# Kernel optimization log

Measured on AMD Instinct MI355X. Metric: run time of the kernel, lower is better.

Reference implementation:

```python
import jax, jax.numpy as jnp
import numpy as np
from jax import lax

B, T, N, C = 32, 32, 64, 64          # batch, window, num_series, inter_dim
GRU_H, QK, HOR = 64, 32, 12          # gru_dim, qk_dim, prediction_horizon
KS = (3, 5, 7)                       # temporal kernel per block (3 + 2*i)


def setup_inputs() -> dict:
    key = jax.random.key(0)
    ks = jax.random.split(key, 32)
    rn = lambda k, shape, s=0.05: jax.random.normal(k, shape, jnp.float32) * s
    inp = {"x": jax.random.normal(ks[0], (B, T, N), jnp.float32)}
    # x_to_inter_dim: Conv1d(1, C, kernel_size=1) == scalar * w + b
    inp["w_x2i"] = rn(ks[1], (C,)); inp["b_x2i"] = rn(ks[2], (C,))
    # latentCorrelation GRU (input_size=1, hidden=GRU_H), gate order r,z,n
    inp["gru_wih"] = rn(ks[3], (3 * GRU_H, 1)); inp["gru_whh"] = rn(ks[4], (3 * GRU_H, GRU_H))
    inp["gru_bih"] = rn(ks[5], (3 * GRU_H,)); inp["gru_bhh"] = rn(ks[6], (3 * GRU_H,))
    inp["wq_w"] = rn(ks[7], (QK, GRU_H)); inp["wq_b"] = rn(ks[8], (QK,))
    inp["wk_w"] = rn(ks[9], (QK, GRU_H)); inp["wk_b"] = rn(ks[10], (QK,))
    # per block: T independent GCNConvs (theta + bias), one temporal Conv1d
    for i, k_ in enumerate(KS):
        inp[f"gcn_w{i}"] = rn(ks[11 + 4 * i], (T, C, C))
        inp[f"gcn_b{i}"] = rn(ks[12 + 4 * i], (T, C))
        inp[f"conv_w{i}"] = rn(ks[13 + 4 * i], (C, C, k_))
        inp[f"conv_b{i}"] = rn(ks[14 + 4 * i], (C,))
    inp["lout_w"] = rn(ks[25], (N * HOR, T * N * C), 0.01)
    inp["lout_b"] = rn(ks[26], (N * HOR,))
    return inp


def _forward(x, w_x2i, b_x2i, gru_wih, gru_whh, gru_bih, gru_bhh,
             wq_w, wq_b, wk_w, wk_b,
             gcn_w0, gcn_b0, conv_w0, conv_b0,
             gcn_w1, gcn_b1, conv_w1, conv_b1,
             gcn_w2, gcn_b2, conv_w2, conv_b2,
             lout_w, lout_b):
    xs = jnp.transpose(x, (1, 0, 2))  # (T, B, N) time-major

    # --- latentCorrelation: one GRU run over all B*N series at once ---
    def gru_step(h, xt):  # h: (B,N,GRU_H), xt: (B,N)
        gi = xt[..., None] * gru_wih[:, 0] + gru_bih           # (B,N,3H)
        gh = h @ gru_whh.T + gru_bhh                           # (B,N,3H)
        r = jax.nn.sigmoid(gi[..., :GRU_H] + gh[..., :GRU_H])
        z = jax.nn.sigmoid(gi[..., GRU_H:2 * GRU_H] + gh[..., GRU_H:2 * GRU_H])
        n = jnp.tanh(gi[..., 2 * GRU_H:] + r * gh[..., 2 * GRU_H:])
        return (1.0 - z) * n + z * h, None

    h0 = jnp.zeros((B, N, GRU_H), x.dtype)
    hT, _ = lax.scan(gru_step, h0, xs)                         # (B,N,GRU_H)
    Q = hT @ wq_w.T + wq_b                                     # (B,N,QK)
    K = hT @ wk_w.T + wk_b
    Wadj = jax.nn.softmax(jnp.einsum('bnq,bmq->bnm', Q, K) / jnp.sqrt(jnp.float32(QK)), axis=2)

    # GCN symmetric norm on the dense complete graph; edge (src=i, tgt=j) has
    # weight Wadj[b,i,j]; degree is per-target (column) sum.
    deg = Wadj.sum(axis=1)                                     # (B,N)
    dinv = jnp.where(deg > 0, 1.0 / jnp.sqrt(deg), 0.0)
    What = dinv[:, :, None] * Wadj * dinv[:, None, :]          # (B,N,N)

    # x_to_inter_dim (1x1 conv) applied per timestep
    feats = xs[..., None] * w_x2i + b_x2i                      # (T,B,N,C)

    for gw, gb, cw, cb, k_ in ((gcn_w0, gcn_b0, conv_w0, conv_b0, 3),
                               (gcn_w1, gcn_b1, conv_w1, conv_b1, 5),
                               (gcn_w2, gcn_b2, conv_w2, conv_b2, 7)):
        xw = jnp.einsum('tbnc,tcd->tbnd', feats, gw)           # per-timestep theta
        agg = jnp.einsum('bij,tbid->tbjd', What, xw) + gb[:, None, None, :]
        seq = jnp.transpose(agg, (1, 2, 3, 0)).reshape(B * N, C, T)
        p = k_ // 2
        conv = lax.conv_general_dilated(seq, cw, (1,), [(p, p)],
                                        dimension_numbers=('NCH', 'OIH', 'NCH'))
        conv = conv + cb[None, :, None]
        conv = jnp.where(conv >= 0, conv, 0.01 * conv)         # LeakyReLU (dropout p=0)
        feats = jnp.transpose(conv.reshape(B, N, C, T), (3, 0, 1, 2))

    # stack(x_list, dim=2).view(B*N, C*T).view(B, -1) -> (B, N*C*T) feature order (n,c,t)
    flat = jnp.transpose(feats, (1, 2, 3, 0)).reshape(B, N * C * T)
    out = flat @ lout_w.T + lout_b                             # (B, N*HOR)
    return out.reshape(B, HOR, N)


def reference(x, w_x2i, b_x2i, gru_wih, gru_whh, gru_bih, gru_bhh,
              wq_w, wq_b, wk_w, wk_b,
              gcn_w0, gcn_b0, conv_w0, conv_b0,
              gcn_w1, gcn_b1, conv_w1, conv_b1,
              gcn_w2, gcn_b2, conv_w2, conv_b2,
              lout_w, lout_b):
    return _forward(x, w_x2i, b_x2i, gru_wih, gru_whh, gru_bih, gru_bhh,
                    wq_w, wq_b, wk_w, wk_b,
                    gcn_w0, gcn_b0, conv_w0, conv_b0,
                    gcn_w1, gcn_b1, conv_w1, conv_b1,
                    gcn_w2, gcn_b2, conv_w2, conv_b2,
                    lout_w, lout_b)
```

## Files before the change

kernel.cpp:

```cpp
#include <hip/hip_runtime.h>
#include <hip/hip_bf16.h>

#define BB 32
#define TT 32
#define NN 64
#define CC 64
#define HH 64
#define QKD 32
#define HOR 12
#define OUTD (NN*HOR)
#define KFLAT (NN*CC*TT)

typedef __attribute__((ext_vector_type(4))) float f32x4;
typedef __attribute__((ext_vector_type(8))) short s16x8;
typedef unsigned short ush;

static __device__ __forceinline__ ush f2bf(float f) {
    unsigned u = __float_as_uint(f);
    unsigned r = (u + 0x7FFFu + ((u >> 16) & 1u)) >> 16;
    return (ush)r;
}
static __device__ __forceinline__ float bf2f(ush h) {
    return __uint_as_float(((unsigned)h) << 16);
}
static __device__ __forceinline__ void split8(const float* f, uint4& hi, uint4& lo) {
    unsigned hh[8], ll[8];
    #pragma unroll
    for (int i = 0; i < 8; ++i) {
        ush h = f2bf(f[i]);
        float hf = bf2f(h);
        hh[i] = h;
        ll[i] = f2bf(f[i] - hf);
    }
    hi = make_uint4(hh[0] | (hh[1] << 16), hh[2] | (hh[3] << 16),
                    hh[4] | (hh[5] << 16), hh[6] | (hh[7] << 16));
    lo = make_uint4(ll[0] | (ll[1] << 16), ll[2] | (ll[3] << 16),
                    ll[4] | (ll[5] << 16), ll[6] | (ll[7] << 16));
}
static __device__ __forceinline__ void gl2lds16(const void* gsrc, void* ldst) {
    __builtin_amdgcn_global_load_lds(
        (const __attribute__((address_space(1))) unsigned int*)gsrc,
        (__attribute__((address_space(3))) unsigned int*)ldst, 16, 0, 0);
}

__global__ __launch_bounds__(256) void prep_gru_kernel(
    const float* __restrict__ x, const float* __restrict__ wih,
    const float* __restrict__ whh, const float* __restrict__ bih,
    const float* __restrict__ bhh, float* __restrict__ hT,
    const float* __restrict__ gw0, const float* __restrict__ wx, const float* __restrict__ bx,
    float* __restrict__ u, float* __restrict__ v,
    const float* __restrict__ gw1, ush* __restrict__ g1h, ush* __restrict__ g1l,
    const float* __restrict__ gw2, ush* __restrict__ g2h, ush* __restrict__ g2l,
    const float* __restrict__ cw1, ush* __restrict__ c1h, ush* __restrict__ c1l,
    const float* __restrict__ cw2, ush* __restrict__ c2h, ush* __restrict__ c2l,
    const float* __restrict__ cw3, ush* __restrict__ c3h, ush* __restrict__ c3l,
    const float* __restrict__ lb, float* __restrict__ out)
{
    __shared__ __align__(16) char smem[17408];
    int bid = blockIdx.x, tid = threadIdx.x;

    if (bid < 32) {
        float (*pu)[64] = (float(*)[64])smem;
        float (*pv)[64] = (float(*)[64])(smem + 1024);
        int t = bid, d = tid & 63, cq = tid >> 6;
        float su = 0.f, sv = 0.f;
        for (int c = cq*16; c < cq*16 + 16; ++c) {
            float gv = gw0[t*4096 + c*64 + d];
            su += wx[c]*gv; sv += bx[c]*gv;
        }
        pu[cq][d] = su; pv[cq][d] = sv;
        __syncthreads();
        if (tid < 64) {
            u[t*64 + tid] = pu[0][tid]+pu[1][tid]+pu[2][tid]+pu[3][tid];
            v[t*64 + tid] = pv[0][tid]+pv[1][tid]+pv[2][tid]+pv[3][tid];
        }
    } else if (bid < 96) {
        const float* gw = (bid < 64) ? gw1 : gw2;
        ush* hi = (bid < 64) ? g1h : g2h;
        ush* lo = (bid < 64) ? g1l : g2l;
        int t = (bid < 64) ? bid - 32 : bid - 64;
        for (int idx = tid; idx < 4096; idx += 256) {
            int d = idx >> 6, c = idx & 63;
            float val = gw[t*4096 + c*64 + d];
            ush h = f2bf(val);
            hi[t*4096 + idx] = h;
            lo[t*4096 + idx] = f2bf(val - bf2f(h));
        }
    } else if (bid < 224) {
        const float* cw; ush *hi, *lo; int KW, co;
        if (bid < 160) { cw = cw2; hi = c2h; lo = c2l; KW = 5; co = bid - 96; }
        else           { cw = cw3; hi = c3h; lo = c3l; KW = 7; co = bid - 160; }
        int K = KW*64;
        for (int idx = tid; idx < K; idx += 256) {
            int ka = idx >> 6, ci = idx & 63;
            float val = cw[(size_t)(co*64 + ci)*KW + ka];
            ush h = f2bf(val);
            hi[(size_t)co*K + idx] = h;
            lo[(size_t)co*K + idx] = f2bf(val - bf2f(h));
        }
    } else if (bid < 288) {
        const float* cw = cw1; ush *hi = c1h, *lo = c1l; int KW = 3, co = bid - 224;
        int K = KW*64;
        for (int idx = tid; idx < K; idx += 256) {
            int ka = idx >> 6, ci = idx & 63;
            float val = cw[(size_t)(co*64 + ci)*KW + ka];
            ush h = f2bf(val);
            hi[(size_t)co*K + idx] = h;
            lo[(size_t)co*K + idx] = f2bf(val - bf2f(h));
        }
    } else if (bid < 384) {
        int idx = (bid - 288)*256 + tid;
        out[idx] = lb[idx % OUTD];
    }
    __syncthreads();

    {
        float (*hbuf)[64] = (float(*)[64])smem;
        float4* part = (float4*)(smem + 1024);
        int w = tid >> 6, j = tid & 63;
        float Wreg[3][16];
        #pragma unroll
        for (int g = 0; g < 3; ++g)
            #pragma unroll
            for (int q = 0; q < 4; ++q) {
                float4 wv = *(const float4*)&whh[(g*64 + j)*64 + w*16 + q*4];
                Wreg[g][q*4+0] = wv.x; Wreg[g][q*4+1] = wv.y;
                Wreg[g][q*4+2] = wv.z; Wreg[g][q*4+3] = wv.w;
            }
        hbuf[w][j] = 0.0f;
        int gs0 = bid * 4;
        int b = gs0 >> 6, n0 = gs0 & 63;
        float wih_r = wih[j], wih_z = wih[64+j], wih_n = wih[128+j];
        float bi_r = bih[j], bi_z = bih[64+j], bi_n = bih[128+j];
        float bh_r = bhh[j], bh_z = bhh[64+j], bh_n = bhh[128+j];
        __syncthreads();
        float hreg = 0.0f;
        for (int t = 0; t < TT; ++t) {
            float p[3][4];
            #pragma unroll
            for (int g = 0; g < 3; ++g)
                #pragma unroll
                for (int s = 0; s < 4; ++s) p[g][s] = 0.f;
            #pragma unroll
            for (int s = 0; s < 4; ++s) {
                #pragma unroll
                for (int q = 0; q < 4; ++q) {
                    const float4 hv = *(const float4*)&hbuf[s][w*16 + q*4];
                    #pragma unroll
                    for (int g = 0; g < 3; ++g) {
                        p[g][s] += hv.x*Wreg[g][q*4]   + hv.y*Wreg[g][q*4+1]
                                 + hv.z*Wreg[g][q*4+2] + hv.w*Wreg[g][q*4+3];
                    }
                }
            }
            #pragma unroll
            for (int s = 0; s < 4; ++s)
                part[(w*4 + s)*64 + j] = make_float4(p[0][s], p[1][s], p[2][s], 0.f);
            __syncthreads();
            float4 q0 = part[(0*4 + w)*64 + j];
            float4 q1 = part[(1*4 + w)*64 + j];
            float4 q2 = part[(2*4 + w)*64 + j];
            float4 q3 = part[(3*4 + w)*64 + j];
            float gr = bh_r + q0.x + q1.x + q2.x + q3.x;
            float gz = bh_z + q0.y + q1.y + q2.y + q3.y;
            float gn = bh_n + q0.z + q1.z + q2.z + q3.z;
            float xt = x[(b*TT + t)*NN + n0 + w];
            float r = 1.f/(1.f+__expf(-(xt*wih_r + bi_r + gr)));
            float z = 1.f/(1.f+__expf(-(xt*wih_z + bi_z + gz)));
            float nn_ = tanhf(xt*wih_n + bi_n + r*gn);
            float hnew = (1.f - z)*nn_ + z*hreg;
            hreg = hnew;
            hbuf[w][j] = hnew;
            __syncthreads();
        }
        hT[(gs0 + w)*64 + j] = hreg;
    }
}

__global__ __launch_bounds__(256) void attn_kernel(
    const float* __restrict__ hT, const float* __restrict__ wq_w,
    const float* __restrict__ wq_b, const float* __restrict__ wk_w,
    const float* __restrict__ wk_b,
    ush* __restrict__ whT_hi, ush* __restrict__ whT_lo)
{
    __shared__ float hs[64][64];
    __shared__ float Qs[64][33], Ks[64][33];
    __shared__ float S[64][65];
    __shared__ float pd[4][64];
    __shared__ float dinv[64];
    int b = blockIdx.x, tid = threadIdx.x;
    for (int idx = tid; idx < 64*64; idx += 256) hs[idx>>6][idx&63] = hT[b*4096 + idx];
    __syncthreads();
    for (int idx = tid; idx < 64*32; idx += 256) {
        int n_ = idx >> 5, q = idx & 31;
        float accq = wq_b[q], acck = wk_b[q];
        #pragma unroll 8
        for (int h_ = 0; h_ < 64; ++h_) {
            float hv = hs[n_][h_];
            accq += hv * wq_w[q*64 + h_];
            acck += hv * wk_w[q*64 + h_];
        }
        Qs[n_][q] = accq; Ks[n_][q] = acck;
    }
    __syncthreads();
    const float scale = 0.17677669529663687f;
    for (int idx = tid; idx < 64*64; idx += 256) {
        int n_ = idx >> 6, m = idx & 63;
        float acc = 0.f;
        #pragma unroll 8
        for (int q = 0; q < 32; ++q) acc += Qs[n_][q]*Ks[m][q];
        S[n_][m] = acc * scale;
    }
    __syncthreads();
    {
        int r = tid >> 2, q = tid & 3;
        float mx = -1e30f;
        #pragma unroll
        for (int m = 0; m < 16; ++m) mx = fmaxf(mx, S[r][q*16+m]);
        mx = fmaxf(mx, __shfl_xor(mx, 1));
        mx = fmaxf(mx, __shfl_xor(mx, 2));
        float sum = 0.f;
        float e[16];
        #pragma unroll
        for (int m = 0; m < 16; ++m) { e[m] = __expf(S[r][q*16+m]-mx); sum += e[m]; }
        sum += __shfl_xor(sum, 1);
        sum += __shfl_xor(sum, 2);
        float inv = 1.f/sum;
        #pragma unroll
        for (int m = 0; m < 16; ++m) S[r][q*16+m] = e[m]*inv;
    }
    __syncthreads();
    {
        int c = tid & 63, rq = tid >> 6;
        float d = 0.f;
        #pragma unroll
        for (int i = 0; i < 16; ++i) d += S[rq*16 + i][c];
        pd[rq][c] = d;
    }
    __syncthreads();
    if (tid < 64) {
        float d = pd[0][tid]+pd[1][tid]+pd[2][tid]+pd[3][tid];
        dinv[tid] = (d > 0.f) ? 1.0f/sqrtf(d) : 0.f;
    }
    __syncthreads();
    for (int idx = tid; idx < 64*64; idx += 256) {
        int jj = idx >> 6, ii = idx & 63;
        float val = dinv[ii]*S[ii][jj]*dinv[jj];
        ush h = f2bf(val);
        whT_hi[b*4096 + idx] = h;
        whT_lo[b*4096 + idx] = f2bf(val - bf2f(h));
    }
}

template<bool FIRST>
__global__ __launch_bounds__(256) void gcn_mfma(
    const float* __restrict__ fin,
    const ush* __restrict__ gwT_hi, const ush* __restrict__ gwT_lo,
    const float* __restrict__ u, const float* __restrict__ v,
    const ush* __restrict__ whT_hi, const ush* __restrict__ whT_lo,
    const float* __restrict__ gb, float* __restrict__ o)
{
    __shared__ __align__(16) ush ft_hi[64][64], ft_lo[64][64];
    __shared__ __align__(16) ush xsT_hi[64][64], xsT_lo[64][64];
    __shared__ float x_l[64];
    int tb = blockIdx.x, t = tb >> 5, b = tb & 31;
    int tid = threadIdx.x;
    int w = tid >> 6, l = tid & 63, lm = l & 15, ld = l >> 4;

    if (FIRST) {
        if (tid < 64) x_l[tid] = fin[(b*TT + t)*NN + tid];
        __syncthreads();
        int d = tid >> 2, nq = tid & 3;
        float ud = u[t*64 + d], vd = v[t*64 + d];
        float vals[16];
        #pragma unroll
        for (int i = 0; i < 16; ++i) vals[i] = x_l[nq*16 + i]*ud + vd;
        #pragma unroll
        for (int h = 0; h < 2; ++h) {
            uint4 hi, lo; split8(&vals[h*8], hi, lo);
            int un = (nq*2 + h) ^ (d & 7);
            *(uint4*)&xsT_hi[d][un*8] = hi;
            *(uint4*)&xsT_lo[d][un*8] = lo;
        }
        __syncthreads();
    } else {
        {
            int row = tid >> 2, c0 = (tid & 3) * 16;
            const float* src = fin + (size_t)tb*4096 + row*64 + c0;
            float f8a[8], f8b[8];
            *(float4*)f8a = *(const float4*)src;       *(float4*)(f8a+4) = *(const float4*)(src+4);
            *(float4*)f8b = *(const float4*)(src+8);   *(float4*)(f8b+4) = *(const float4*)(src+12);
            uint4 hi, lo;
            split8(f8a, hi, lo);
            int u0 = ((c0>>3)) ^ (row & 7);
            *(uint4*)&ft_hi[row][u0*8] = hi; *(uint4*)&ft_lo[row][u0*8] = lo;
            split8(f8b, hi, lo);
            int u1 = ((c0>>3)+1) ^ (row & 7);
            *(uint4*)&ft_hi[row][u1*8] = hi; *(uint4*)&ft_lo[row][u1*8] = lo;
        }
        __syncthreads();
        f32x4 acc[4];
        #pragma unroll
        for (int ct = 0; ct < 4; ++ct) acc[ct] = (f32x4){0.f,0.f,0.f,0.f};
        #pragma unroll
        for (int kc = 0; kc < 2; ++kc) {
            int nrow = w*16 + lm;
            int ux = (kc*4 + ld) ^ (nrow & 7);
            s16x8 xh = *(const s16x8*)&ft_hi[nrow][ux*8];
            s16x8 xl = *(const s16x8*)&ft_lo[nrow][ux*8];
            #pragma unroll
            for (int ct = 0; ct < 4; ++ct) {
                int drow = ct*16 + lm;
                s16x8 yh = *(const s16x8*)&gwT_hi[t*4096 + drow*64 + kc*32 + ld*8];
                s16x8 yl = *(const s16x8*)&gwT_lo[t*4096 + drow*64 + kc*32 + ld*8];
                acc[ct] = __builtin_amdgcn_mfma_f32_16x16x32_bf16(xh, yh, acc[ct], 0, 0, 0);
                acc[ct] = __builtin_amdgcn_mfma_f32_16x16x32_bf16(xh, yl, acc[ct], 0, 0, 0);
                acc[ct] = __builtin_amdgcn_mfma_f32_16x16x32_bf16(xl, yh, acc[ct], 0, 0, 0);
            }
        }
        #pragma unroll
        for (int ct = 0; ct < 4; ++ct) {
            int d = ct*16 + lm;
            int n0 = w*16 + ld*4;
            ush hh[4], llo[4];
            #pragma unroll
            for (int r = 0; r < 4; ++r) {
                float val = acc[ct][r];
                ush h = f2bf(val);
                hh[r] = h; llo[r] = f2bf(val - bf2f(h));
            }
            int un = (n0 >> 3) ^ (d & 7);
            int base = d*64 + un*8 + (n0 & 7);
            *(uint2*)&xsT_hi[0][0 + base] = make_uint2(hh[0]|(hh[1]<<16), hh[2]|(hh[3]<<16));
            *(uint2*)&xsT_lo[0][0 + base] = make_uint2(llo[0]|(llo[1]<<16), llo[2]|(llo[3]<<16));
        }
        __syncthreads();
    }

    f32x4 acc2[4];
    #pragma unroll
    for (int ct = 0; ct < 4; ++ct) acc2[ct] = (f32x4){0.f,0.f,0.f,0.f};
    #pragma unroll
    for (int kc = 0; kc < 2; ++kc) {
        int jrow = w*16 + lm;
        s16x8 wh = *(const s16x8*)&whT_hi[b*4096 + jrow*64 + kc*32 + ld*8];
        s16x8 wl = *(const s16x8*)&whT_lo[b*4096 + jrow*64 + kc*32 + ld*8];
        #pragma unroll
        for (int ct = 0; ct < 4; ++ct) {
            int drow = ct*16 + lm;
            int uy = (kc*4 + ld) ^ (drow & 7);
            s16x8 yh = *(const s16x8*)&xsT_hi[drow][uy*8];
            s16x8 yl = *(const s16x8*)&xsT_lo[drow][uy*8];
            acc2[ct] = __builtin_amdgcn_mfma_f32_16x16x32_bf16(wh, yh, acc2[ct], 0, 0, 0);
            acc2[ct] = __builtin_amdgcn_mfma_f32_16x16x32_bf16(wh, yl, acc2[ct], 0, 0, 0);
            acc2[ct] = __builtin_amdgcn_mfma_f32_16x16x32_bf16(wl, yh, acc2[ct], 0, 0, 0);
        }
    }
    float* oo = o + (size_t)tb*4096;
    #pragma unroll
    for (int ct = 0; ct < 4; ++ct) {
        int d = ct*16 + lm;
        float bias = gb[t*64 + d];
        #pragma unroll
        for (int r = 0; r < 4; ++r) {
            int jj = w*16 + ld*4 + r;
            oo[jj*64 + d] = acc2[ct][r] + bias;
        }
    }
}

template<int KW, bool LAST>
__global__ __launch_bounds__(256) void conv_mfma(float* __restrict__ g,
    const ush* __restrict__ wch, const ush* __restrict__ wcl,
    const float* __restrict__ cb, ush* __restrict__ fo)
{
    constexpr int P = KW/2, K = KW*64, K32 = KW*2;
    __shared__ __align__(16) ush sh[32][64], sl[32][64];
    int bn = blockIdx.x, tid = threadIdx.x;
    {
        int t = tid >> 3, c0 = (tid & 7) * 8;
        const float* src = &g[((size_t)t*2048 + bn)*64 + c0];
        float f8[8];
        *(float4*)f8 = *(const float4*)src;
        *(float4*)(f8+4) = *(const float4*)(src+4);
        uint4 hi, lo; split8(f8, hi, lo);
        int uu = (tid & 7) ^ (t & 7);
        *(uint4*)&sh[t][uu*8] = hi;
        *(uint4*)&sl[t][uu*8] = lo;
    }
    __syncthreads();
    int w = tid >> 6, l = tid & 63, lm = l & 15, ld = l >> 4;
    int co = w*16 + lm;
    f32x4 acc0 = {0.f,0.f,0.f,0.f}, acc1 = {0.f,0.f,0.f,0.f};
    const s16x8 zf = {0,0,0,0,0,0,0,0};
    for (int kc = 0; kc < K32; ++kc) {
        int ka = kc >> 1;
        int ci = (kc & 1)*32 + ld*8;
        s16x8 yh = *(const s16x8*)&wch[(size_t)co*K + kc*32 + ld*8];
        s16x8 yl = *(const s16x8*)&wcl[(size_t)co*K + kc*32 + ld*8];
        #pragma unroll
        for (int Mt = 0; Mt < 2; ++Mt) {
            int ts = Mt*16 + lm + ka - P;
            bool ok = ((unsigned)ts) < 32u;
            int tc = ok ? ts : 0;
            int ua = (ci >> 3) ^ (tc & 7);
            s16x8 xh = *(const s16x8*)&sh[tc][ua*8];
            s16x8 xl = *(const s16x8*)&sl[tc][ua*8];
            if (!ok) { xh = zf; xl = zf; }
            f32x4& a = Mt ? acc1 : acc0;
            a = __builtin_amdgcn_mfma_f32_16x16x32_bf16(xh, yh, a, 0, 0, 0);
            a = __builtin_amdgcn_mfma_f32_16x16x32_bf16(xh, yl, a, 0, 0, 0);
            a = __builtin_amdgcn_mfma_f32_16x16x32_bf16(xl, yh, a, 0, 0, 0);
        }
    }
    float bias = cb[co];
    if (LAST) {
        int b = bn >> 6, n = bn & 63;
        ush* ob = fo + (size_t)b*KFLAT + n*2048 + co*32;
        #pragma unroll
        for (int Mt = 0; Mt < 2; ++Mt) {
            const f32x4& a = Mt ? acc1 : acc0;
            ush hv[4];
            #pragma unroll
            for (int r = 0; r < 4; ++r) {
                float val = a[r] + bias;
                val = (val >= 0.f) ? val : 0.01f*val;
                hv[r] = f2bf(val);
            }
            *(uint2*)&ob[Mt*16 + ld*4] = make_uint2(hv[0]|(hv[1]<<16), hv[2]|(hv[3]<<16));
        }
    } else {
        #pragma unroll
        for (int Mt = 0; Mt < 2; ++Mt) {
            const f32x4& a = Mt ? acc1 : acc0;
            #pragma unroll
            for (int r = 0; r < 4; ++r) {
                int t = Mt*16 + ld*4 + r;
                float val = a[r] + bias;
                val = (val >= 0.f) ? val : 0.01f*val;
                g[((size_t)t*2048 + bn)*64 + co] = val;
            }
        }
    }
}

__global__ __launch_bounds__(256) void gemm_mfma(const ush* __restrict__ flat,
                                                 const float* __restrict__ W,
                                                 float* __restrict__ out)
{
    __shared__ __align__(16) float Wl[3][64][64];
    __shared__ __align__(16) ush Al[3][32][64];
    const int tid = threadIdx.x;
    const int w = tid >> 6, l = tid & 63;
    const int og = blockIdx.x >> 6;
    const int kc = blockIdx.x & 63;
    const int o_blk = og * 64;
    const int kbase = kc * 2048;

    const int wrow_l = l >> 4;
    const int wu = l & 15;
    size_t w_off[4];
    #pragma unroll
    for (int i = 0; i < 4; ++i) {
        int row = w*16 + i*4 + wrow_l;
        w_off[i] = (size_t)(o_blk + row) * KFLAT + (unsigned)((wu ^ (row & 7)) * 4);
    }
    const int arow = w*8 + (l >> 3);
    const int au = l & 7;
    const size_t a_off0 = (size_t)arow * KFLAT + (unsigned)((au ^ (arow & 7)) * 8);

#define ISSUE_TILE(buf_, s_) { \
    int kwin_ = kbase + (s_)*64; \
    _Pragma("unroll") \
    for (int i_ = 0; i_ < 4; ++i_) \
        gl2lds16(W + w_off[i_] + kwin_, &Wl[buf_][w*16 + i_*4][0]); \
    gl2lds16(flat + a_off0 + kwin_, &Al[buf_][w*8][0]); \
}

    f32x4 acc0 = {0.f,0.f,0.f,0.f}, acc1 = {0.f,0.f,0.f,0.f};
    ISSUE_TILE(0, 0);
    ISSUE_TILE(1, 1);
    ISSUE_TILE(2, 2);

    const int lmod = l & 15, ldiv = l >> 4, lx = l & 7;
    int cur = 0;
    for (int s = 0; s < 32; ++s) {
        if (s < 30)      { asm volatile("s_waitcnt vmcnt(10)" ::: "memory"); }
        else if (s == 30){ asm volatile("s_waitcnt vmcnt(5)" ::: "memory"); }
        else             { asm volatile("s_waitcnt vmcnt(0)" ::: "memory"); }
        __builtin_amdgcn_s_barrier();
        asm volatile("" ::: "memory");
        #pragma unroll
        for (int ksub = 0; ksub < 2; ++ksub) {
            int ju = ksub*8 + ldiv*2;
            const float4 b0 = *(const float4*)&Wl[cur][w*16 + lmod][(ju ^ lx)*4];
            const float4 b1 = *(const float4*)&Wl[cur][w*16 + lmod][((ju+1) ^ lx)*4];
            float bf[8] = {b0.x,b0.y,b0.z,b0.w,b1.x,b1.y,b1.z,b1.w};
            s16x8 bhi;
            #pragma unroll
            for (int i = 0; i < 8; ++i) bhi[i] = (short)f2bf(bf[i]);
            int jua = ksub*4 + ldiv;
            const s16x8 a0 = *(const s16x8*)&Al[cur][lmod]      [(jua ^ lx)*8];
            const s16x8 a1 = *(const s16x8*)&Al[cur][16 + lmod] [(jua ^ lx)*8];
            acc0 = __builtin_amdgcn_mfma_f32_16x16x32_bf16(a0, bhi, acc0, 0, 0, 0);
            acc1 = __builtin_amdgcn_mfma_f32_16x16x32_bf16(a1, bhi, acc1, 0, 0, 0);
        }
        asm volatile("" ::: "memory");
        __builtin_amdgcn_s_barrier();
        if (s < 29) { ISSUE_TILE(cur, s+3); }
        cur = (cur == 2) ? 0 : cur + 1;
    }
#undef ISSUE_TILE

    const int o_out = o_blk + w*16 + lmod;
    #pragma unroll
    for (int r = 0; r < 4; ++r) {
        int b0_ = ldiv*4 + r;
        atomicAdd(&out[(size_t)b0_*OUTD + o_out], acc0[r]);
        atomicAdd(&out[(size_t)(16 + b0_)*OUTD + o_out], acc1[r]);
    }
}

extern "C" void kernel_launch(void* const* d_in, const int* in_sizes, int n_in,
                              void* d_out, int out_size, void* d_ws, size_t ws_size,
                              hipStream_t stream) {
    (void)in_sizes; (void)n_in; (void)out_size; (void)ws_size;
    const float* x        = (const float*)d_in[0];
    const float* w_x2i    = (const float*)d_in[1];
    const float* b_x2i    = (const float*)d_in[2];
    const float* gru_wih  = (const float*)d_in[3];
    const float* gru_whh  = (const float*)d_in[4];
    const float* gru_bih  = (const float*)d_in[5];
    const float* gru_bhh  = (const float*)d_in[6];
    const float* wq_w     = (const float*)d_in[7];
    const float* wq_b     = (const float*)d_in[8];
    const float* wk_w     = (const float*)d_in[9];
    const float* wk_b     = (const float*)d_in[10];
    const float* gcn_w[3]  = {(const float*)d_in[11], (const float*)d_in[15], (const float*)d_in[19]};
    const float* gcn_b[3]  = {(const float*)d_in[12], (const float*)d_in[16], (const float*)d_in[20]};
    const float* conv_w[3] = {(const float*)d_in[13], (const float*)d_in[17], (const float*)d_in[21]};
    const float* conv_b[3] = {(const float*)d_in[14], (const float*)d_in[18], (const float*)d_in[22]};
    const float* lout_w   = (const float*)d_in[23];
    const float* lout_b   = (const float*)d_in[24];
    float* out = (float*)d_out;
    float* ws  = (float*)d_ws;

    float* hT   = ws;
    float* u    = ws + 131072;
    float* v    = ws + 133120;
    float* bufA = ws + 135168;
    float* bufB = bufA + 4194304;
    ush* usb = (ush*)(ws + 8523776);
    ush* whT_hi  = usb;
    ush* whT_lo  = usb + 131072;
    ush* gwT1_hi = usb + 262144;
    ush* gwT1_lo = usb + 393216;
    ush* gwT2_hi = usb + 524288;
    ush* gwT2_lo = usb + 655360;
    ush* cw2_hi  = usb + 786432;
    ush* cw2_lo  = usb + 806912;
    ush* cw3_hi  = usb + 827392;
    ush* cw3_lo  = usb + 856064;
    ush* cw1_hi  = usb + 884736;
    ush* cw1_lo  = usb + 897024;

    prep_gru_kernel<<<dim3(512), dim3(256), 0, stream>>>(
        x, gru_wih, gru_whh, gru_bih, gru_bhh, hT,
        gcn_w[0], w_x2i, b_x2i, u, v,
        gcn_w[1], gwT1_hi, gwT1_lo,
        gcn_w[2], gwT2_hi, gwT2_lo,
        conv_w[0], cw1_hi, cw1_lo,
        conv_w[1], cw2_hi, cw2_lo,
        conv_w[2], cw3_hi, cw3_lo,
        lout_b, out);
    attn_kernel<<<dim3(32), dim3(256), 0, stream>>>(hT, wq_w, wq_b, wk_w, wk_b, whT_hi, whT_lo);

    unsigned short* flat16 = (unsigned short*)bufB;
    gcn_mfma<true><<<dim3(1024), dim3(256), 0, stream>>>(x, nullptr, nullptr, u, v,
                                                         whT_hi, whT_lo, gcn_b[0], bufA);
    conv_mfma<3,false><<<dim3(2048), dim3(256), 0, stream>>>(bufA, cw1_hi, cw1_lo, conv_b[0], nullptr);
    gcn_mfma<false><<<dim3(1024), dim3(256), 0, stream>>>(bufA, gwT1_hi, gwT1_lo, u, v,
                                                          whT_hi, whT_lo, gcn_b[1], bufB);
    conv_mfma<5,false><<<dim3(2048), dim3(256), 0, stream>>>(bufB, cw2_hi, cw2_lo, conv_b[1], nullptr);
    gcn_mfma<false><<<dim3(1024), dim3(256), 0, stream>>>(bufB, gwT2_hi, gwT2_lo, u, v,
                                                          whT_hi, whT_lo, gcn_b[2], bufA);
    conv_mfma<7,true><<<dim3(2048), dim3(256), 0, stream>>>(bufA, cw3_hi, cw3_lo, conv_b[2], flat16);

    gemm_mfma<<<dim3(768), dim3(256), 0, stream>>>(flat16, lout_w, out);
}
```

Baseline: 308.1 us.

## Pre-convert output weights to bf16 inside earlier kernels to halve final GEMM traffic

```diff
diff --git a/kernel.cpp b/kernel.cpp
--- a/kernel.cpp
+++ b/kernel.cpp
@@ -10,6 +10,7 @@
 #define HOR 12
 #define OUTD (NN*HOR)
 #define KFLAT (NN*CC*TT)
+#define WTOT4 25165824u
 
 typedef __attribute__((ext_vector_type(4))) float f32x4;
 typedef __attribute__((ext_vector_type(8))) short s16x8;
@@ -41,6 +42,17 @@
     __builtin_amdgcn_global_load_lds(
         (const __attribute__((address_space(1))) unsigned int*)gsrc,
         (__attribute__((address_space(3))) unsigned int*)ldst, 16, 0, 0);
+}
+
+static __device__ void convW(const float* __restrict__ W, ush* __restrict__ wbf,
+                             unsigned s4, unsigned e4, unsigned gtid, unsigned stride) {
+    const float4* W4 = (const float4*)W;
+    for (unsigned i = s4 + gtid; i < e4; i += stride) {
+        float4 w = W4[i];
+        uint2 p = make_uint2((unsigned)f2bf(w.x) | ((unsigned)f2bf(w.y) << 16),
+                             (unsigned)f2bf(w.z) | ((unsigned)f2bf(w.w) << 16));
+        *(uint2*)(wbf + (size_t)i*4) = p;
+    }
 }
 
 __global__ __launch_bounds__(256) void prep_gru_kernel(
@@ -54,10 +66,13 @@
     const float* __restrict__ cw1, ush* __restrict__ c1h, ush* __restrict__ c1l,
     const float* __restrict__ cw2, ush* __restrict__ c2h, ush* __restrict__ c2l,
     const float* __restrict__ cw3, ush* __restrict__ c3h, ush* __restrict__ c3l,
-    const float* __restrict__ lb, float* __restrict__ out)
+    const float* __restrict__ lb, float* __restrict__ out,
+    const float* __restrict__ W, ush* __restrict__ wbf, unsigned cs, unsigned ce)
 {
     __shared__ __align__(16) char smem[17408];
     int bid = blockIdx.x, tid = threadIdx.x;
+    bool cfirst = (bid & 1);
+    if (cfirst) convW(W, wbf, cs, ce, bid*256 + tid, 512*256);
 
     if (bid < 32) {
         float (*pu)[64] = (float(*)[64])smem;
@@ -175,20 +190,26 @@
         }
         hT[(gs0 + w)*64 + j] = hreg;
     }
+    if (!cfirst) convW(W, wbf, cs, ce, bid*256 + tid, 512*256);
 }
 
 __global__ __launch_bounds__(256) void attn_kernel(
     const float* __restrict__ hT, const float* __restrict__ wq_w,
     const float* __restrict__ wq_b, const float* __restrict__ wk_w,
     const float* __restrict__ wk_b,
-    ush* __restrict__ whT_hi, ush* __restrict__ whT_lo)
+    ush* __restrict__ whT_hi, ush* __restrict__ whT_lo,
+    const float* __restrict__ W, ush* __restrict__ wbf, unsigned cs, unsigned ce)
 {
+    int b = blockIdx.x, tid = threadIdx.x;
+    if (b >= 32) {
+        convW(W, wbf, cs, ce, (b - 32)*256 + tid, 480*256);
+        return;
+    }
     __shared__ float hs[64][64];
     __shared__ float Qs[64][33], Ks[64][33];
     __shared__ float S[64][65];
     __shared__ float pd[4][64];
     __shared__ float dinv[64];
-    int b = blockIdx.x, tid = threadIdx.x;
     for (int idx = tid; idx < 64*64; idx += 256) hs[idx>>6][idx&63] = hT[b*4096 + idx];
     __syncthreads();
     for (int idx = tid; idx < 64*32; idx += 256) {
@@ -258,7 +279,8 @@
     const ush* __restrict__ gwT_hi, const ush* __restrict__ gwT_lo,
     const float* __restrict__ u, const float* __restrict__ v,
     const ush* __restrict__ whT_hi, const ush* __restrict__ whT_lo,
-    const float* __restrict__ gb, float* __restrict__ o)
+    const float* __restrict__ gb, float* __restrict__ o,
+    const float* __restrict__ W, ush* __restrict__ wbf, unsigned cs, unsigned ce)
 {
     __shared__ __align__(16) ush ft_hi[64][64], ft_lo[64][64];
     __shared__ __align__(16) ush xsT_hi[64][64], xsT_lo[64][64];
@@ -266,6 +288,8 @@
     int tb = blockIdx.x, t = tb >> 5, b = tb & 31;
     int tid = threadIdx.x;
     int w = tid >> 6, l = tid & 63, lm = l & 15, ld = l >> 4;
+    bool cfirst = (tb & 1);
+    if (cfirst) convW(W, wbf, cs, ce, tb*256 + tid, 1024*256);
 
     if (FIRST) {
         if (tid < 64) x_l[tid] = fin[(b*TT + t)*NN + tid];
@@ -367,16 +391,20 @@
             oo[jj*64 + d] = acc2[ct][r] + bias;
         }
     }
+    if (!cfirst) convW(W, wbf, cs, ce, tb*256 + tid, 1024*256);
 }
 
 template<int KW, bool LAST>
 __global__ __launch_bounds__(256) void conv_mfma(float* __restrict__ g,
     const ush* __restrict__ wch, const ush* __restrict__ wcl,
-    const float* __restrict__ cb, ush* __restrict__ fo)
+    const float* __restrict__ cb, ush* __restrict__ fo,
+    const float* __restrict__ W, ush* __restrict__ wbf, unsigned cs, unsigned ce)
 {
     constexpr int P = KW/2, K = KW*64, K32 = KW*2;
     __shared__ __align__(16) ush sh[32][64], sl[32][64];
     int bn = blockIdx.x, tid = threadIdx.x;
+    bool cfirst = (bn & 1);
+    if (cfirst && cs < ce) convW(W, wbf, cs, ce, bn*256 + tid, 2048*256);
     {
         int t = tid >> 3, c0 = (tid & 7) * 8;
         const float* src = &g[((size_t)t*2048 + bn)*64 + c0];
@@ -442,13 +470,14 @@
             }
         }
     }
+    if (!cfirst && cs < ce) convW(W, wbf, cs, ce, bn*256 + tid, 2048*256);
 }
 
 __global__ __launch_bounds__(256) void gemm_mfma(const ush* __restrict__ flat,
-                                                 const float* __restrict__ W,
+                                                 const ush* __restrict__ wbf,
                                                  float* __restrict__ out)
 {
-    __shared__ __align__(16) float Wl[3][64][64];
+    __shared__ __align__(16) ush Wl[3][64][64];
     __shared__ __align__(16) ush Al[3][32][64];
     const int tid = threadIdx.x;
     const int w = tid >> 6, l = tid & 63;
@@ -457,13 +486,12 @@
     const int o_blk = og * 64;
     const int kbase = kc * 2048;
 
-    const int wrow_l = l >> 4;
-    const int wu = l & 15;
-    size_t w_off[4];
+    size_t w_off[2];
     #pragma unroll
-    for (int i = 0; i < 4; ++i) {
-        int row = w*16 + i*4 + wrow_l;
-        w_off[i] = (size_t)(o_blk + row) * KFLAT + (unsigned)((wu ^ (row & 7)) * 4);
+    for (int i = 0; i < 2; ++i) {
+        int wrow = w*16 + i*8 + (l >> 3);
+        int wu = l & 7;
+        w_off[i] = (size_t)(o_blk + wrow) * KFLAT + (unsigned)((wu ^ (wrow & 7)) * 8);
     }
     const int arow = w*8 + (l >> 3);
     const int au = l & 7;
@@ -471,9 +499,8 @@
 
 #define ISSUE_TILE(buf_, s_) { \
     int kwin_ = kbase + (s_)*64; \
-    _Pragma("unroll") \
-    for (int i_ = 0; i_ < 4; ++i_) \
-        gl2lds16(W + w_off[i_] + kwin_, &Wl[buf_][w*16 + i_*4][0]); \
+    gl2lds16(wbf + w_off[0] + kwin_, &Wl[buf_][w*16][0]); \
+    gl2lds16(wbf + w_off[1] + kwin_, &Wl[buf_][w*16 + 8][0]); \
     gl2lds16(flat + a_off0 + kwin_, &Al[buf_][w*8][0]); \
 }
 
@@ -485,23 +512,17 @@
     const int lmod = l & 15, ldiv = l >> 4, lx = l & 7;
     int cur = 0;
     for (int s = 0; s < 32; ++s) {
-        if (s < 30)      { asm volatile("s_waitcnt vmcnt(10)" ::: "memory"); }
-        else if (s == 30){ asm volatile("s_waitcnt vmcnt(5)" ::: "memory"); }
+        if (s < 30)      { asm volatile("s_waitcnt vmcnt(6)" ::: "memory"); }
+        else if (s == 30){ asm volatile("s_waitcnt vmcnt(3)" ::: "memory"); }
         else             { asm volatile("s_waitcnt vmcnt(0)" ::: "memory"); }
         __builtin_amdgcn_s_barrier();
         asm volatile("" ::: "memory");
         #pragma unroll
         for (int ksub = 0; ksub < 2; ++ksub) {
-            int ju = ksub*8 + ldiv*2;
-            const float4 b0 = *(const float4*)&Wl[cur][w*16 + lmod][(ju ^ lx)*4];
-            const float4 b1 = *(const float4*)&Wl[cur][w*16 + lmod][((ju+1) ^ lx)*4];
-            float bf[8] = {b0.x,b0.y,b0.z,b0.w,b1.x,b1.y,b1.z,b1.w};
-            s16x8 bhi;
-            #pragma unroll
-            for (int i = 0; i < 8; ++i) bhi[i] = (short)f2bf(bf[i]);
-            int jua = ksub*4 + ldiv;
-            const s16x8 a0 = *(const s16x8*)&Al[cur][lmod]      [(jua ^ lx)*8];
-            const s16x8 a1 = *(const s16x8*)&Al[cur][16 + lmod] [(jua ^ lx)*8];
+            int ju = ksub*4 + ldiv;
+            const s16x8 bhi = *(const s16x8*)&Wl[cur][w*16 + lmod][(ju ^ lx)*8];
+            const s16x8 a0  = *(const s16x8*)&Al[cur][lmod]      [(ju ^ lx)*8];
+            const s16x8 a1  = *(const s16x8*)&Al[cur][16 + lmod] [(ju ^ lx)*8];
             acc0 = __builtin_amdgcn_mfma_f32_16x16x32_bf16(a0, bhi, acc0, 0, 0, 0);
             acc1 = __builtin_amdgcn_mfma_f32_16x16x32_bf16(a1, bhi, acc1, 0, 0, 0);
         }
@@ -563,6 +584,12 @@
     ush* cw3_lo  = usb + 856064;
     ush* cw1_hi  = usb + 884736;
     ush* cw1_lo  = usb + 897024;
+    ush* wbf     = usb + 909312;
+
+    unsigned sb[8];
+    for (int i = 0; i < 8; ++i)
+        sb[i] = (unsigned)((unsigned long long)WTOT4 * i / 7u);
+    sb[7] = WTOT4;
 
     prep_gru_kernel<<<dim3(512), dim3(256), 0, stream>>>(
         x, gru_wih, gru_whh, gru_bih, gru_bhh, hT,
@@ -572,19 +599,28 @@
         conv_w[0], cw1_hi, cw1_lo,
         conv_w[1], cw2_hi, cw2_lo,
         conv_w[2], cw3_hi, cw3_lo,
-        lout_b, out);
-    attn_kernel<<<dim3(32), dim3(256), 0, stream>>>(hT, wq_w, wq_b, wk_w, wk_b, whT_hi, whT_lo);
+        lout_b, out,
+        lout_w, wbf, sb[0], sb[1]);
+    attn_kernel<<<dim3(512), dim3(256), 0, stream>>>(
+        hT, wq_w, wq_b, wk_w, wk_b, whT_hi, whT_lo,
+        lout_w, wbf, sb[1], sb[2]);
 
     unsigned short* flat16 = (unsigned short*)bufB;
     gcn_mfma<true><<<dim3(1024), dim3(256), 0, stream>>>(x, nullptr, nullptr, u, v,
-                                                         whT_hi, whT_lo, gcn_b[0], bufA);
-    conv_mfma<3,false><<<dim3(2048), dim3(256), 0, stream>>>(bufA, cw1_hi, cw1_lo, conv_b[0], nullptr);
+                                                         whT_hi, whT_lo, gcn_b[0], bufA,
+                                                         lout_w, wbf, sb[2], sb[3]);
+    conv_mfma<3,false><<<dim3(2048), dim3(256), 0, stream>>>(bufA, cw1_hi, cw1_lo, conv_b[0], nullptr,
+                                                             lout_w, wbf, sb[3], sb[4]);
     gcn_mfma<false><<<dim3(1024), dim3(256), 0, stream>>>(bufA, gwT1_hi, gwT1_lo, u, v,
-                                                          whT_hi, whT_lo, gcn_b[1], bufB);
-    conv_mfma<5,false><<<dim3(2048), dim3(256), 0, stream>>>(bufB, cw2_hi, cw2_lo, conv_b[1], nullptr);
+                                                          whT_hi, whT_lo, gcn_b[1], bufB,
+                                                          lout_w, wbf, sb[4], sb[5]);
+    conv_mfma<5,false><<<dim3(2048), dim3(256), 0, stream>>>(bufB, cw2_hi, cw2_lo, conv_b[1], nullptr,
+                                                             lout_w, wbf, sb[5], sb[6]);
     gcn_mfma<false><<<dim3(1024), dim3(256), 0, stream>>>(bufB, gwT2_hi, gwT2_lo, u, v,
-                                                          whT_hi, whT_lo, gcn_b[2], bufA);
-    conv_mfma<7,true><<<dim3(2048), dim3(256), 0, stream>>>(bufA, cw3_hi, cw3_lo, conv_b[2], flat16);
-
-    gemm_mfma<<<dim3(768), dim3(256), 0, stream>>>(flat16, lout_w, out);
-}
+                                                          whT_hi, whT_lo, gcn_b[2], bufA,
+                                                          lout_w, wbf, sb[6], sb[7]);
+    conv_mfma<7,true><<<dim3(2048), dim3(256), 0, stream>>>(bufA, cw3_hi, cw3_lo, conv_b[2], flat16,
+                                                            lout_w, wbf, 0u, 0u);
+
+    gemm_mfma<<<dim3(768), dim3(256), 0, stream>>>(flat16, wbf, out);
+}
```

Result: slower. 357.9 us (+16.2%).
